# Kernel tuning notes

Measured on AMD Instinct MI355X. Metric: run time of the kernel, lower is better.

## Reference

```python
import jax, jax.numpy as jnp
import numpy as np

B, N, H = 16, 1024, 1024


def setup_inputs() -> dict:
    key = jax.random.key(0)
    ks = jax.random.split(key, 12)
    inv = 1.0 / np.sqrt(H)
    inp = {
        "x": jax.random.normal(ks[0], (B, N, H), jnp.float32),
        "atom_graph": jax.random.normal(ks[1], (B, N, N), jnp.float32),
        "variable_graph": jax.random.normal(ks[2], (B, N, N), jnp.float32),
        "Wq": jax.random.uniform(ks[3], (H, H), jnp.float32, -inv, inv),
        "bq": jax.random.uniform(ks[4], (H,), jnp.float32, -inv, inv),
        "Wk": jax.random.uniform(ks[5], (H, H), jnp.float32, -inv, inv),
        "bk": jax.random.uniform(ks[6], (H,), jnp.float32, -inv, inv),
        "Wv": jax.random.uniform(ks[7], (H, H), jnp.float32, -inv, inv),
        "bv": jax.random.uniform(ks[8], (H,), jnp.float32, -inv, inv),
        "predicate_pos": jax.random.randint(ks[9], (B, N), 0, 2, jnp.int32),
        "variable_tags": jax.random.randint(ks[10], (B, N), 0, 4, jnp.int32),
    }
    return inp


def _path_pool(h, predicate_pos):
    # h: [B,N,H]; predicate_pos: [B,N] in {0,1}
    b, n, d = h.shape
    i = jnp.arange(n)
    # pos[i-2] (value irrelevant for i<2, those branches handled explicitly)
    pp2 = jnp.pad(predicate_pos, ((0, 0), (2, 0)))[:, :n]  # [B,N]
    # window [s, e): i==0 -> [0,2); i==1 -> [0,3); pos[i-2]==1 -> [i,i+2); else [i-1,i+2)
    s = jnp.where(i < 2, 0, jnp.where(pp2 == 1, i, i - 1))  # [B,N]
    e = jnp.where(i == 0, 2, jnp.where(i == 1, 3, i + 2))    # [N]
    e = jnp.minimum(e, n)
    e = jnp.broadcast_to(e, (b, n))
    # prefix sums along node dim with a leading zero row -> windowed means via gather
    cs = jnp.concatenate([jnp.zeros((b, 1, d), h.dtype), jnp.cumsum(h, axis=1)], axis=1)  # [B,N+1,H]
    win_sum = (jnp.take_along_axis(cs, e[:, :, None], axis=1)
               - jnp.take_along_axis(cs, s[:, :, None], axis=1))  # [B,N,H]
    means = win_sum / (e - s)[:, :, None].astype(h.dtype)
    mask = (predicate_pos == 1).astype(h.dtype)  # [B,N]
    item = (means * mask[:, :, None]).sum(axis=1) / mask.sum(axis=1)[:, None]  # [B,H]
    return jnp.broadcast_to(item[:, None, :], (b, n, d))


def reference(x, atom_graph, variable_graph, Wq, bq, Wk, bk, Wv, bv,
              predicate_pos, variable_tags):
    scale = x.shape[-1] ** (-0.5)
    q = (x @ Wq.T + bq) * scale
    k = x @ Wk.T + bk
    v = x @ Wv.T + bv
    att = jnp.einsum("bnh,bmh->bnm", q, k) + atom_graph + variable_graph
    att = jax.nn.softmax(att, axis=-1)  # dropout is identity in eval
    h = jnp.einsum("bnm,bmh->bnh", att, v)
    return _path_pool(h, predicate_pos)
```

## Files before the change

### kernel.cpp

```cpp
#include <hip/hip_runtime.h>
#include <hip/hip_bf16.h>

#define BATCH 16
#define SEQ   1024
#define DIM   1024

typedef __attribute__((ext_vector_type(8))) short bf16x8;
typedef __attribute__((ext_vector_type(4))) float f32x4;
typedef __attribute__((ext_vector_type(4))) unsigned short us4;

__device__ __forceinline__ float bfu2f(unsigned short u) {
  union { unsigned int i; float f; } c; c.i = ((unsigned int)u) << 16; return c.f;
}
__device__ __forceinline__ unsigned short f2bfu(float f) {
  union { float f; unsigned int i; } c; c.f = f;
  return (unsigned short)((c.i + 0x7FFFu + ((c.i >> 16) & 1u)) >> 16);
}
__device__ __forceinline__ void async16(void* lds, const void* g) {
  __builtin_amdgcn_global_load_lds(
      (const __attribute__((address_space(1))) unsigned int*)g,
      (__attribute__((address_space(3))) unsigned int*)lds, 16, 0, 0);
}

__global__ void cast_xw_kernel(const float* __restrict__ x, const float* __restrict__ Wv,
                               unsigned short* __restrict__ xb,
                               unsigned short* __restrict__ Wvb, int x4) {
  int i = blockIdx.x * blockDim.x + threadIdx.x;
  const float* in; unsigned short* out; int j;
  if (i < x4) { in = x; out = xb; j = i; }
  else { in = Wv; out = Wvb; j = i - x4; }
  f32x4 v = ((const f32x4*)in)[j];
  us4 o;
  o[0] = f2bfu(v[0]); o[1] = f2bfu(v[1]); o[2] = f2bfu(v[2]); o[3] = f2bfu(v[3]);
  ((us4*)out)[j] = o;
}

__global__ void castT_kernel(const float* __restrict__ Wq, const float* __restrict__ Wk,
                             unsigned short* __restrict__ WqT,
                             unsigned short* __restrict__ WkT) {
  const float* in = (blockIdx.z == 0) ? Wq : Wk;
  unsigned short* out = (blockIdx.z == 0) ? WqT : WkT;
  __shared__ float t[64][65];
  const int h0 = blockIdx.x * 64, i0 = blockIdx.y * 64;
  const int tid = threadIdx.x;
  const int sub = tid >> 4, c4 = tid & 15;
#pragma unroll
  for (int p = 0; p < 4; ++p) {
    const int row = p * 16 + sub;
    f32x4 v = *(const f32x4*)(in + (size_t)(h0 + row) * DIM + i0 + c4 * 4);
    t[row][c4 * 4 + 0] = v[0]; t[row][c4 * 4 + 1] = v[1];
    t[row][c4 * 4 + 2] = v[2]; t[row][c4 * 4 + 3] = v[3];
  }
  __syncthreads();
#pragma unroll
  for (int p = 0; p < 4; ++p) {
    const int orow = p * 16 + sub;
    us4 o;
    o[0] = f2bfu(t[c4 * 4 + 0][orow]);
    o[1] = f2bfu(t[c4 * 4 + 1][orow]);
    o[2] = f2bfu(t[c4 * 4 + 2][orow]);
    o[3] = f2bfu(t[c4 * 4 + 3][orow]);
    *(us4*)(out + (size_t)(i0 + orow) * DIM + h0 + c4 * 4) = o;
  }
}

__global__ void t12_kernel(const unsigned short* __restrict__ WqT,
                           const unsigned short* __restrict__ WkT,
                           const float* __restrict__ bq, const float* __restrict__ bk,
                           float* __restrict__ t1, float* __restrict__ t2) {
  const int y = blockIdx.y;
  const unsigned short* Wt = y ? WkT : WqT;
  const float* vec = y ? bq : bk;
  float* tout = y ? t2 : t1;
  const int wave = threadIdx.x >> 6, lane = threadIdx.x & 63;
  const int i = blockIdx.x * 4 + wave;
  const us4* wr = (const us4*)(Wt + (size_t)i * DIM);
  float s = 0.f;
#pragma unroll
  for (int t = 0; t < 4; ++t) {
    us4 w4 = wr[lane + 64 * t];
    f32x4 b4 = *(const f32x4*)(vec + (lane + 64 * t) * 4);
    s += bfu2f(w4[0]) * b4[0] + bfu2f(w4[1]) * b4[1] +
         bfu2f(w4[2]) * b4[2] + bfu2f(w4[3]) * b4[3];
  }
#pragma unroll
  for (int o = 32; o; o >>= 1) s += __shfl_down(s, o);
  if (lane == 0) tout[i] = s;
}

__global__ void ac_kernel(const unsigned short* __restrict__ xb,
                          const float* __restrict__ t1, const float* __restrict__ t2,
                          const float* __restrict__ bq, const float* __restrict__ bk,
                          float* __restrict__ a, float* __restrict__ c) {
  const float scale = 0.03125f;
  const int tid = threadIdx.x;
  const int wave = tid >> 6, lane = tid & 63;
  float dp = 0.f;
  for (int i = tid; i < DIM; i += 256) dp += bq[i] * bk[i];
#pragma unroll
  for (int o = 32; o; o >>= 1) dp += __shfl_down(dp, o);
  __shared__ float dred[4];
  if ((tid & 63) == 0) dred[tid >> 6] = dp;
  __syncthreads();
  const float d = dred[0] + dred[1] + dred[2] + dred[3];
  float t1r[16], t2r[16];
#pragma unroll
  for (int t = 0; t < 4; ++t) {
    f32x4 v1 = *(const f32x4*)(t1 + (lane + 64 * t) * 4);
    f32x4 v2 = *(const f32x4*)(t2 + (lane + 64 * t) * 4);
#pragma unroll
    for (int j = 0; j < 4; ++j) { t1r[t * 4 + j] = v1[j]; t2r[t * 4 + j] = v2[j]; }
  }
  for (int rr = 0; rr < 16; ++rr) {
    const int row = blockIdx.x * 64 + wave * 16 + rr;
    const us4* xr = (const us4*)(xb + (size_t)row * DIM);
    float sa = 0.f, sc = 0.f;
#pragma unroll
    for (int t = 0; t < 4; ++t) {
      us4 v = xr[lane + 64 * t];
#pragma unroll
      for (int j = 0; j < 4; ++j) {
        const float f = bfu2f(v[j]);
        sa += f * t1r[t * 4 + j];
        sc += f * t2r[t * 4 + j];
      }
    }
#pragma unroll
    for (int o = 32; o; o >>= 1) { sa += __shfl_down(sa, o); sc += __shfl_down(sc, o); }
    if (lane == 0) {
      a[row] = scale * (sa + d);
      c[row] = scale * sc;
    }
  }
}

__global__ void pathw_kernel(const int* __restrict__ pos, float* __restrict__ w,
                             float* __restrict__ zbias) {
  const int b = blockIdx.x;
  __shared__ int ps[SEQ];
  __shared__ int mcnt;
  const int tid = threadIdx.x;
  if (tid == 0) mcnt = 0;
  __syncthreads();
  if (b == 0)
    for (int i = tid; i < DIM; i += 256) zbias[i] = 0.f;
  for (int i = tid; i < SEQ; i += 256) ps[i] = pos[b * SEQ + i];
  __syncthreads();
  int c = 0;
  for (int i = tid; i < SEQ; i += 256) c += ps[i];
  for (int o = 32; o; o >>= 1) c += __shfl_down(c, o);
  if ((tid & 63) == 0) atomicAdd(&mcnt, c);
  __syncthreads();
  const float invM = 1.0f / (float)mcnt;
  for (int j = tid; j < SEQ; j += 256) {
    float a = 0.f;
#pragma unroll
    for (int di = -1; di <= 1; ++di) {
      int i = j + di;
      if (i < 0 || i >= SEQ) continue;
      if (!ps[i]) continue;
      int s, e;
      if (i < 2) { s = 0; e = (i == 0) ? 2 : 3; }
      else { s = (ps[i - 2] == 1) ? i : (i - 1); e = i + 2; if (e > SEQ) e = SEQ; }
      if (s <= j && j < e) a += 1.0f / (float)(e - s);
    }
    w[b * SEQ + j] = a * invM;
  }
}

__global__ void proj_gemm(const unsigned short* __restrict__ A,
                          const unsigned short* __restrict__ W,
                          const float* __restrict__ bias, float alpha,
                          unsigned short* __restrict__ C, int M, int N, int K)
{
  __shared__ __align__(16) char smem[32768];
  float* Sl = (float*)smem;
  const int tid = threadIdx.x;
  const int wave = tid >> 6, lane = tid & 63;
  const int lr = lane & 15, lg = lane >> 4;
  const int wr = wave >> 1, wc = wave & 1;
  const int flat = blockIdx.x + gridDim.x * blockIdx.y;
  const int q8 = (gridDim.x * gridDim.y) >> 3;
  const int t = (flat & 7) * q8 + (flat >> 3);
  const int m0 = (t / gridDim.y) * 128;
  const int n0 = (t % gridDim.y) * 128;
  const int off0 = tid * 16, off1 = 4096 + tid * 16;
  const int r0 = off0 >> 6, ke0 = (off0 >> 1) & 31;
  const int r1 = off1 >> 6, ke1 = (off1 >> 1) & 31;
  f32x4 acc[4][4] = {};

  auto stage = [&](char* base, int kk) {
    async16(base + off0, A + (size_t)(m0 + r0) * K + kk + ke0);
    async16(base + off1, A + (size_t)(m0 + r1) * K + kk + ke1);
    async16(base + 8192 + off0, W + (size_t)(n0 + r0) * K + kk + ke0);
    async16(base + 8192 + off1, W + (size_t)(n0 + r1) * K + kk + ke1);
  };
  auto compute = [&](const char* base) {
    bf16x8 af[4], bfv[4];
#pragma unroll
    for (int i = 0; i < 4; ++i) {
      af[i]  = *(const bf16x8*)(base + ((wr * 64 + i * 16 + lr) << 6) + (lg << 4));
      bfv[i] = *(const bf16x8*)(base + 8192 + ((wc * 64 + i * 16 + lr) << 6) + (lg << 4));
    }
#pragma unroll
    for (int i = 0; i < 4; ++i)
#pragma unroll
      for (int j = 0; j < 4; ++j)
        acc[i][j] = __builtin_amdgcn_mfma_f32_16x16x32_bf16(af[i], bfv[j], acc[i][j], 0, 0, 0);
  };

  const int nt = K >> 5;
  stage(smem, 0);
  __syncthreads();
  int cur = 0;
  for (int k = 0; k < nt - 1; ++k) {
    stage(smem + ((cur ^ 1) << 14), (k + 1) << 5);
    compute(smem + (cur << 14));
    __syncthreads();
    cur ^= 1;
  }
  compute(smem + (cur << 14));
#pragma unroll
  for (int p = 0; p < 4; ++p) {
    __syncthreads();
    if (wr == (p >> 1)) {
      const int ibase = (p & 1) * 2;
#pragma unroll
      for (int ii = 0; ii < 2; ++ii) {
        const int i = ibase + ii;
#pragma unroll
        for (int j = 0; j < 4; ++j)
#pragma unroll
          for (int r = 0; r < 4; ++r)
            Sl[(ii * 16 + lg * 4 + r) * 132 + wc * 64 + j * 16 + lr] = acc[i][j][r];
      }
    }
    __syncthreads();
#pragma unroll
    for (int it = 0; it < 4; ++it) {
      const int v = tid + it * 256;
      const int lrow = v >> 5, c4 = v & 31;
      const int grow = m0 + p * 32 + lrow;
      const int col = n0 + c4 * 4;
      const f32x4 s4 = *(const f32x4*)(&Sl[lrow * 132 + c4 * 4]);
      const f32x4 b4 = *(const f32x4*)(bias + col);
      us4 o;
      o[0] = f2bfu((s4[0] + b4[0]) * alpha);
      o[1] = f2bfu((s4[1] + b4[1]) * alpha);
      o[2] = f2bfu((s4[2] + b4[2]) * alpha);
      o[3] = f2bfu((s4[3] + b4[3]) * alpha);
      *(us4*)(C + (size_t)grow * N + col) = o;
    }
  }
}

__global__ void sgemm_kernel(const unsigned short* __restrict__ z,
                             const unsigned short* __restrict__ xb,
                             unsigned short* __restrict__ S)
{
  __shared__ __align__(16) char smem[33792];
  unsigned short* Slb = (unsigned short*)smem;
  const int flat = blockIdx.x + 8 * blockIdx.y + 64 * blockIdx.z;
  const int t = (flat & 7) * 128 + (flat >> 3);
  const int b = t >> 6;
  const int m0 = (t & 7) * 128;
  const int n0 = ((t >> 3) & 7) * 128;
  const unsigned short* Aq = z + ((size_t)b << 20);
  const unsigned short* Bk = xb + ((size_t)b << 20);
  const int tid = threadIdx.x;
  const int wave = tid >> 6, lane = tid & 63;
  const int lr = lane & 15, lg = lane >> 4;
  const int wr = wave >> 1, wc = wave & 1;
  const int off0 = tid * 16, off1 = 4096 + tid * 16;
  const int r0 = off0 >> 6, ke0 = (off0 >> 1) & 31;
  const int r1 = off1 >> 6, ke1 = (off1 >> 1) & 31;
  f32x4 acc[4][4] = {};

  auto stage = [&](char* base, int kk) {
    async16(base + off0, Aq + (size_t)(m0 + r0) * DIM + kk + ke0);
    async16(base + off1, Aq + (size_t)(m0 + r1) * DIM + kk + ke1);
    async16(base + 8192 + off0, Bk + (size_t)(n0 + r0) * DIM + kk + ke0);
    async16(base + 8192 + off1, Bk + (size_t)(n0 + r1) * DIM + kk + ke1);
  };
  auto compute = [&](const char* base) {
    bf16x8 af[4], bfv[4];
#pragma unroll
    for (int i = 0; i < 4; ++i) {
      af[i]  = *(const bf16x8*)(base + ((wr * 64 + i * 16 + lr) << 6) + (lg << 4));
      bfv[i] = *(const bf16x8*)(base + 8192 + ((wc * 64 + i * 16 + lr) << 6) + (lg << 4));
    }
#pragma unroll
    for (int i = 0; i < 4; ++i)
#pragma unroll
      for (int j = 0; j < 4; ++j)
        acc[i][j] = __builtin_amdgcn_mfma_f32_16x16x32_bf16(af[i], bfv[j], acc[i][j], 0, 0, 0);
  };

  stage(smem, 0);
  __syncthreads();
  int cur = 0;
  for (int k = 0; k < 31; ++k) {
    stage(smem + ((cur ^ 1) << 14), (k + 1) << 5);
    compute(smem + (cur << 14));
    __syncthreads();
    cur ^= 1;
  }
  compute(smem + (cur << 14));
  __syncthreads();
#pragma unroll
  for (int i = 0; i < 4; ++i)
#pragma unroll
    for (int j = 0; j < 4; ++j)
#pragma unroll
      for (int r = 0; r < 4; ++r)
        Slb[(wr * 64 + i * 16 + lg * 4 + r) * 132 + wc * 64 + j * 16 + lr] =
            f2bfu(acc[i][j][r]);
  __syncthreads();
  unsigned short* Sb = S + ((size_t)b << 20);
#pragma unroll
  for (int it = 0; it < 16; ++it) {
    const int v = tid + it * 256;
    const int lrow = v >> 5, c4 = v & 31;
    *(us4*)(Sb + (size_t)(m0 + lrow) * SEQ + n0 + c4 * 4) =
        *(const us4*)(&Slb[lrow * 132 + c4 * 4]);
  }
}

__global__ void exp_kernel(unsigned short* __restrict__ SE,
                           const float* __restrict__ ag, const float* __restrict__ vg,
                           const float* __restrict__ av, const float* __restrict__ cv,
                           float* __restrict__ denom)
{
  const int b = blockIdx.y;
  const int wave = threadIdx.x >> 6, lane = threadIdx.x & 63;
  const int r0 = blockIdx.x * 8 + wave * 2;
  const float* agb = ag + ((size_t)b << 20);
  const float* vgb = vg + ((size_t)b << 20);
  const float* cvb = cv + b * SEQ;
  unsigned short* Eb = SE + ((size_t)b << 20);
#pragma unroll
  for (int r = 0; r < 2; ++r) {
    const int row = r0 + r;
    const float arow = av[b * SEQ + row];
    us4 sv[4]; f32x4 a4[4], g4[4], cq[4];
#pragma unroll
    for (int qi = 0; qi < 4; ++qi) {
      const int col = (lane + 64 * qi) * 4;
      const size_t base = (size_t)row * SEQ + col;
      sv[qi] = *(const us4*)(Eb + base);
      a4[qi] = *(const f32x4*)(agb + base);
      g4[qi] = *(const f32x4*)(vgb + base);
      cq[qi] = *(const f32x4*)(cvb + col);
    }
    float rs = 0.f;
#pragma unroll
    for (int qi = 0; qi < 4; ++qi) {
      const int col = (lane + 64 * qi) * 4;
      const size_t base = (size_t)row * SEQ + col;
      const float e0 = __expf(bfu2f(sv[qi][0]) + a4[qi][0] + g4[qi][0] + arow + cq[qi][0]);
      const float e1 = __expf(bfu2f(sv[qi][1]) + a4[qi][1] + g4[qi][1] + arow + cq[qi][1]);
      const float e2 = __expf(bfu2f(sv[qi][2]) + a4[qi][2] + g4[qi][2] + arow + cq[qi][2]);
      const float e3 = __expf(bfu2f(sv[qi][3]) + a4[qi][3] + g4[qi][3] + arow + cq[qi][3]);
      us4 o;
      o[0] = f2bfu(e0); o[1] = f2bfu(e1); o[2] = f2bfu(e2); o[3] = f2bfu(e3);
      *(us4*)(Eb + base) = o;
      rs += e0 + e1 + e2 + e3;
    }
#pragma unroll
    for (int o2 = 32; o2; o2 >>= 1) rs += __shfl_down(rs, o2);
    if (lane == 0) denom[b * SEQ + row] = rs;
  }
}

__global__ void wcol_kernel(const unsigned short* __restrict__ Mt,
                            const float* __restrict__ wv,
                            const float* __restrict__ dv,
                            float* __restrict__ part) {
  const int nc = blockIdx.x;
  const int b = blockIdx.y;
  const int tid = threadIdx.x;
  __shared__ float c[64];
  if (tid < 64) {
    const int n = nc * 64 + tid;
    float cvw = wv[b * SEQ + n];
    if (dv) cvw /= dv[b * SEQ + n];
    c[tid] = cvw;
  }
  __syncthreads();
  const unsigned short* p = Mt + ((size_t)b << 20) + ((size_t)(nc * 64) << 10) + tid * 4;
  f32x4 acc = {0.f, 0.f, 0.f, 0.f};
#pragma unroll 8
  for (int n = 0; n < 64; ++n) {
    const us4 v = *(const us4*)(p + ((size_t)n << 10));
    const float cn = c[n];
    acc[0] += cn * bfu2f(v[0]); acc[1] += cn * bfu2f(v[1]);
    acc[2] += cn * bfu2f(v[2]); acc[3] += cn * bfu2f(v[3]);
  }
  *(f32x4*)(part + (size_t)((b * 16 + nc) << 10) + tid * 4) = acc;
}

__global__ void wred_kernel(const float* __restrict__ part, float* __restrict__ vec,
                            float* __restrict__ su) {
  const int b = blockIdx.x;
  const int tid = threadIdx.x;
  f32x4 s = {0.f, 0.f, 0.f, 0.f};
#pragma unroll
  for (int nc = 0; nc < 16; ++nc) {
    const f32x4 v = *(const f32x4*)(part + (size_t)((b * 16 + nc) << 10) + tid * 4);
    s[0] += v[0]; s[1] += v[1]; s[2] += v[2]; s[3] += v[3];
  }
  *(f32x4*)(vec + b * SEQ + tid * 4) = s;
  if (su) {
    float ts = s[0] + s[1] + s[2] + s[3];
#pragma unroll
    for (int o = 32; o; o >>= 1) ts += __shfl_down(ts, o);
    __shared__ float red[4];
    if ((tid & 63) == 0) red[tid >> 6] = ts;
    __syncthreads();
    if (tid == 0) su[b] = red[0] + red[1] + red[2] + red[3];
  }
}

__global__ void item_kernel(const float* __restrict__ y, const float* __restrict__ su,
                            const unsigned short* __restrict__ Wvb,
                            const float* __restrict__ bv, float* __restrict__ item) {
  const int b = blockIdx.x;
  const int hblk = blockIdx.y;
  __shared__ float ys[DIM];
  const int tid = threadIdx.x;
  for (int i = tid; i < DIM; i += 256) ys[i] = y[b * DIM + i];
  __syncthreads();
  const float sub = su[b];
  const int wave = tid >> 6, lane = tid & 63;
  const int h = hblk * 4 + wave;
  const us4* wrow = (const us4*)(Wvb + (size_t)h * DIM);
  float acc = 0.f;
#pragma unroll
  for (int t = 0; t < 4; ++t) {
    us4 v = wrow[t * 64 + lane];
    const int d0 = (t * 64 + lane) * 4;
    acc += ys[d0] * bfu2f(v[0]) + ys[d0 + 1] * bfu2f(v[1]) +
           ys[d0 + 2] * bfu2f(v[2]) + ys[d0 + 3] * bfu2f(v[3]);
  }
  for (int o = 32; o; o >>= 1) acc += __shfl_down(acc, o);
  if (lane == 0) item[b * DIM + h] = acc + sub * bv[h];
}

__global__ void bcast_kernel(const float* __restrict__ item, float* __restrict__ out) {
  const int b = blockIdx.y;
  const int n = blockIdx.x;
  const f32x4* src = (const f32x4*)(item + b * DIM);
  f32x4* dst = (f32x4*)(out + (((size_t)b * SEQ + n) << 10));
  dst[threadIdx.x] = src[threadIdx.x];
}

extern "C" void kernel_launch(void* const* d_in, const int* in_sizes, int n_in,
                              void* d_out, int out_size, void* d_ws, size_t ws_size,
                              hipStream_t stream) {
  const float* x    = (const float*)d_in[0];
  const float* ag   = (const float*)d_in[1];
  const float* vgr  = (const float*)d_in[2];
  const float* Wq   = (const float*)d_in[3];
  const float* bq   = (const float*)d_in[4];
  const float* Wk   = (const float*)d_in[5];
  const float* bk   = (const float*)d_in[6];
  const float* Wv   = (const float*)d_in[7];
  const float* bv   = (const float*)d_in[8];
  const int*   pos  = (const int*)d_in[9];
  float* out = (float*)d_out;

  char* ws = (char*)d_ws;
  size_t off = 0;
  auto alloc = [&](size_t bytes) { void* p = ws + off; off += (bytes + 255) & ~(size_t)255; return p; };
  const size_t BNH = (size_t)BATCH * SEQ * DIM;
  unsigned short* xb   = (unsigned short*)alloc(BNH * 2);
  unsigned short* zb   = (unsigned short*)alloc(BNH * 2);
  unsigned short* E    = (unsigned short*)alloc(BNH * 2);
  unsigned short* WqT  = (unsigned short*)alloc((size_t)DIM * DIM * 2);
  unsigned short* WkT  = (unsigned short*)alloc((size_t)DIM * DIM * 2);
  unsigned short* Wvb  = (unsigned short*)alloc((size_t)DIM * DIM * 2);
  unsigned short* Hb   = (unsigned short*)alloc((size_t)DIM * DIM * 2);
  float* w     = (float*)alloc((size_t)BATCH * SEQ * 4);
  float* denom = (float*)alloc((size_t)BATCH * SEQ * 4);
  float* u     = (float*)alloc((size_t)BATCH * SEQ * 4);
  float* av    = (float*)alloc((size_t)BATCH * SEQ * 4);
  float* cvv   = (float*)alloc((size_t)BATCH * SEQ * 4);
  float* t1    = (float*)alloc((size_t)DIM * 4);
  float* t2    = (float*)alloc((size_t)DIM * 4);
  float* zbias = (float*)alloc((size_t)DIM * 4);
  float* y     = (float*)alloc((size_t)BATCH * DIM * 4);
  float* su    = (float*)alloc((size_t)BATCH * 4);
  float* item  = (float*)alloc((size_t)BATCH * DIM * 4);
  float* part  = (float*)alloc((size_t)BATCH * 16 * SEQ * 4);

  const float scale = 0.03125f;
  const int x4 = (int)(BNH / 4);

  cast_xw_kernel<<<(x4 + DIM * DIM / 4) / 256, 256, 0, stream>>>(x, Wv, xb, Wvb, x4);
  castT_kernel<<<dim3(16, 16, 2), 256, 0, stream>>>(Wq, Wk, WqT, WkT);

  pathw_kernel<<<BATCH, 256, 0, stream>>>(pos, w, zbias);

  t12_kernel<<<dim3(256, 2), 256, 0, stream>>>(WqT, WkT, bq, bk, t1, t2);
  ac_kernel<<<256, 256, 0, stream>>>(xb, t1, t2, bq, bk, av, cvv);

  proj_gemm<<<dim3(8, 8), 256, 0, stream>>>(WkT, WqT, zbias, scale, Hb, DIM, DIM, DIM);

  proj_gemm<<<dim3(128, 8), 256, 0, stream>>>(xb, Hb, zbias, 1.0f, zb,
                                              BATCH * SEQ, DIM, DIM);

  sgemm_kernel<<<dim3(8, 8, BATCH), 256, 0, stream>>>(zb, xb, E);

  exp_kernel<<<dim3(128, BATCH), 256, 0, stream>>>(E, ag, vgr, av, cvv, denom);

  wcol_kernel<<<dim3(16, BATCH), 256, 0, stream>>>(E, w, denom, part);
  wred_kernel<<<BATCH, 256, 0, stream>>>(part, u, su);

  wcol_kernel<<<dim3(16, BATCH), 256, 0, stream>>>(xb, u, nullptr, part);
  wred_kernel<<<BATCH, 256, 0, stream>>>(part, y, nullptr);

  item_kernel<<<dim3(BATCH, 256), 256, 0, stream>>>(y, su, Wvb, bv, item);

  bcast_kernel<<<dim3(SEQ, BATCH), 256, 0, stream>>>(item, out);
}
```

Measured before the change: 223.5 us.

## Fuse softmax exp with weighted column reduction and skip zero-weight rows

```diff
diff --git a/kernel.cpp b/kernel.cpp
--- a/kernel.cpp
+++ b/kernel.cpp
@@ -135,7 +135,7 @@
 }
 
 __global__ void pathw_kernel(const int* __restrict__ pos, float* __restrict__ w,
-                             float* __restrict__ zbias) {
+                             float* __restrict__ u, float* __restrict__ zbias) {
   const int b = blockIdx.x;
   __shared__ int ps[SEQ];
   __shared__ int mcnt;
@@ -144,7 +144,10 @@
   __syncthreads();
   if (b == 0)
     for (int i = tid; i < DIM; i += 256) zbias[i] = 0.f;
-  for (int i = tid; i < SEQ; i += 256) ps[i] = pos[b * SEQ + i];
+  for (int i = tid; i < SEQ; i += 256) {
+    ps[i] = pos[b * SEQ + i];
+    u[b * SEQ + i] = 0.f;
+  }
   __syncthreads();
   int c = 0;
   for (int i = tid; i < SEQ; i += 256) c += ps[i];
@@ -326,66 +329,86 @@
   }
 }
 
-__global__ void exp_kernel(unsigned short* __restrict__ SE,
-                           const float* __restrict__ ag, const float* __restrict__ vg,
-                           const float* __restrict__ av, const float* __restrict__ cv,
-                           float* __restrict__ denom)
+__global__ void exp_fused_kernel(const unsigned short* __restrict__ S,
+                                 const float* __restrict__ ag, const float* __restrict__ vg,
+                                 const float* __restrict__ av, const float* __restrict__ cv,
+                                 const float* __restrict__ w, float* __restrict__ u)
 {
+  __shared__ float uacc[4][SEQ];
   const int b = blockIdx.y;
-  const int wave = threadIdx.x >> 6, lane = threadIdx.x & 63;
-  const int r0 = blockIdx.x * 8 + wave * 2;
+  const int tid = threadIdx.x;
+  const int wave = tid >> 6, lane = tid & 63;
+  for (int i = tid; i < 4 * SEQ; i += 256) ((float*)uacc)[i] = 0.f;
+  __syncthreads();
   const float* agb = ag + ((size_t)b << 20);
   const float* vgb = vg + ((size_t)b << 20);
+  const unsigned short* Sb = S + ((size_t)b << 20);
   const float* cvb = cv + b * SEQ;
-  unsigned short* Eb = SE + ((size_t)b << 20);
+  f32x4 cq[4];
+#pragma unroll
+  for (int qi = 0; qi < 4; ++qi)
+    cq[qi] = *(const f32x4*)(cvb + (lane + 64 * qi) * 4);
+  const int r0 = blockIdx.x * 8 + wave * 2;
 #pragma unroll
   for (int r = 0; r < 2; ++r) {
     const int row = r0 + r;
+    const float wrow = w[b * SEQ + row];
+    if (wrow == 0.f) continue;
     const float arow = av[b * SEQ + row];
-    us4 sv[4]; f32x4 a4[4], g4[4], cq[4];
+    us4 sv[4]; f32x4 a4[4], g4[4];
+#pragma unroll
+    for (int qi = 0; qi < 4; ++qi) {
+      const size_t base = (size_t)row * SEQ + (lane + 64 * qi) * 4;
+      sv[qi] = *(const us4*)(Sb + base);
+      a4[qi] = *(const f32x4*)(agb + base);
+      g4[qi] = *(const f32x4*)(vgb + base);
+    }
+    float e[16];
+    float rs = 0.f;
+#pragma unroll
+    for (int qi = 0; qi < 4; ++qi)
+#pragma unroll
+      for (int j = 0; j < 4; ++j) {
+        const float ev = __expf(bfu2f(sv[qi][j]) + a4[qi][j] + g4[qi][j] + arow + cq[qi][j]);
+        e[qi * 4 + j] = ev;
+        rs += ev;
+      }
+#pragma unroll
+    for (int o2 = 32; o2; o2 >>= 1) rs += __shfl_xor(rs, o2);
+    const float cn = wrow / rs;
 #pragma unroll
     for (int qi = 0; qi < 4; ++qi) {
       const int col = (lane + 64 * qi) * 4;
-      const size_t base = (size_t)row * SEQ + col;
-      sv[qi] = *(const us4*)(Eb + base);
-      a4[qi] = *(const f32x4*)(agb + base);
-      g4[qi] = *(const f32x4*)(vgb + base);
-      cq[qi] = *(const f32x4*)(cvb + col);
-    }
-    float rs = 0.f;
-#pragma unroll
-    for (int qi = 0; qi < 4; ++qi) {
-      const int col = (lane + 64 * qi) * 4;
-      const size_t base = (size_t)row * SEQ + col;
-      const float e0 = __expf(bfu2f(sv[qi][0]) + a4[qi][0] + g4[qi][0] + arow + cq[qi][0]);
-      const float e1 = __expf(bfu2f(sv[qi][1]) + a4[qi][1] + g4[qi][1] + arow + cq[qi][1]);
-      const float e2 = __expf(bfu2f(sv[qi][2]) + a4[qi][2] + g4[qi][2] + arow + cq[qi][2]);
-      const float e3 = __expf(bfu2f(sv[qi][3]) + a4[qi][3] + g4[qi][3] + arow + cq[qi][3]);
-      us4 o;
-      o[0] = f2bfu(e0); o[1] = f2bfu(e1); o[2] = f2bfu(e2); o[3] = f2bfu(e3);
-      *(us4*)(Eb + base) = o;
-      rs += e0 + e1 + e2 + e3;
-    }
-#pragma unroll
-    for (int o2 = 32; o2; o2 >>= 1) rs += __shfl_down(rs, o2);
-    if (lane == 0) denom[b * SEQ + row] = rs;
-  }
+#pragma unroll
+      for (int j = 0; j < 4; ++j)
+        uacc[wave][col + j] += cn * e[qi * 4 + j];
+    }
+  }
+  __syncthreads();
+  const int col = tid * 4;
+  f32x4 s0 = *(const f32x4*)(&uacc[0][col]);
+  const f32x4 s1 = *(const f32x4*)(&uacc[1][col]);
+  const f32x4 s2 = *(const f32x4*)(&uacc[2][col]);
+  const f32x4 s3 = *(const f32x4*)(&uacc[3][col]);
+  s0[0] += s1[0] + s2[0] + s3[0];
+  s0[1] += s1[1] + s2[1] + s3[1];
+  s0[2] += s1[2] + s2[2] + s3[2];
+  s0[3] += s1[3] + s2[3] + s3[3];
+  float* ub = u + b * SEQ + col;
+  atomicAdd(ub + 0, s0[0]);
+  atomicAdd(ub + 1, s0[1]);
+  atomicAdd(ub + 2, s0[2]);
+  atomicAdd(ub + 3, s0[3]);
 }
 
 __global__ void wcol_kernel(const unsigned short* __restrict__ Mt,
                             const float* __restrict__ wv,
-                            const float* __restrict__ dv,
                             float* __restrict__ part) {
   const int nc = blockIdx.x;
   const int b = blockIdx.y;
   const int tid = threadIdx.x;
   __shared__ float c[64];
-  if (tid < 64) {
-    const int n = nc * 64 + tid;
-    float cvw = wv[b * SEQ + n];
-    if (dv) cvw /= dv[b * SEQ + n];
-    c[tid] = cvw;
-  }
+  if (tid < 64) c[tid] = wv[b * SEQ + nc * 64 + tid];
   __syncthreads();
   const unsigned short* p = Mt + ((size_t)b << 20) + ((size_t)(nc * 64) << 10) + tid * 4;
   f32x4 acc = {0.f, 0.f, 0.f, 0.f};
@@ -399,8 +422,7 @@
   *(f32x4*)(part + (size_t)((b * 16 + nc) << 10) + tid * 4) = acc;
 }
 
-__global__ void wred_kernel(const float* __restrict__ part, float* __restrict__ vec,
-                            float* __restrict__ su) {
+__global__ void wred_kernel(const float* __restrict__ part, float* __restrict__ vec) {
   const int b = blockIdx.x;
   const int tid = threadIdx.x;
   f32x4 s = {0.f, 0.f, 0.f, 0.f};
@@ -410,18 +432,9 @@
     s[0] += v[0]; s[1] += v[1]; s[2] += v[2]; s[3] += v[3];
   }
   *(f32x4*)(vec + b * SEQ + tid * 4) = s;
-  if (su) {
-    float ts = s[0] + s[1] + s[2] + s[3];
-#pragma unroll
-    for (int o = 32; o; o >>= 1) ts += __shfl_down(ts, o);
-    __shared__ float red[4];
-    if ((tid & 63) == 0) red[tid >> 6] = ts;
-    __syncthreads();
-    if (tid == 0) su[b] = red[0] + red[1] + red[2] + red[3];
-  }
-}
-
-__global__ void item_kernel(const float* __restrict__ y, const float* __restrict__ su,
+}
+
+__global__ void item_kernel(const float* __restrict__ y,
                             const unsigned short* __restrict__ Wvb,
                             const float* __restrict__ bv, float* __restrict__ item) {
   const int b = blockIdx.x;
@@ -430,7 +443,6 @@
   const int tid = threadIdx.x;
   for (int i = tid; i < DIM; i += 256) ys[i] = y[b * DIM + i];
   __syncthreads();
-  const float sub = su[b];
   const int wave = tid >> 6, lane = tid & 63;
   const int h = hblk * 4 + wave;
   const us4* wrow = (const us4*)(Wvb + (size_t)h * DIM);
@@ -443,7 +455,7 @@
            ys[d0 + 2] * bfu2f(v[2]) + ys[d0 + 3] * bfu2f(v[3]);
   }
   for (int o = 32; o; o >>= 1) acc += __shfl_down(acc, o);
-  if (lane == 0) item[b * DIM + h] = acc + sub * bv[h];
+  if (lane == 0) item[b * DIM + h] = acc + bv[h];
 }
 
 __global__ void bcast_kernel(const float* __restrict__ item, float* __restrict__ out) {
@@ -475,13 +487,12 @@
   const size_t BNH = (size_t)BATCH * SEQ * DIM;
   unsigned short* xb   = (unsigned short*)alloc(BNH * 2);
   unsigned short* zb   = (unsigned short*)alloc(BNH * 2);
-  unsigned short* E    = (unsigned short*)alloc(BNH * 2);
+  unsigned short* S    = (unsigned short*)alloc(BNH * 2);
   unsigned short* WqT  = (unsigned short*)alloc((size_t)DIM * DIM * 2);
   unsigned short* WkT  = (unsigned short*)alloc((size_t)DIM * DIM * 2);
   unsigned short* Wvb  = (unsigned short*)alloc((size_t)DIM * DIM * 2);
   unsigned short* Hb   = (unsigned short*)alloc((size_t)DIM * DIM * 2);
   float* w     = (float*)alloc((size_t)BATCH * SEQ * 4);
-  float* denom = (float*)alloc((size_t)BATCH * SEQ * 4);
   float* u     = (float*)alloc((size_t)BATCH * SEQ * 4);
   float* av    = (float*)alloc((size_t)BATCH * SEQ * 4);
   float* cvv   = (float*)alloc((size_t)BATCH * SEQ * 4);
@@ -489,7 +500,6 @@
   float* t2    = (float*)alloc((size_t)DIM * 4);
   float* zbias = (float*)alloc((size_t)DIM * 4);
   float* y     = (float*)alloc((size_t)BATCH * DIM * 4);
-  float* su    = (float*)alloc((size_t)BATCH * 4);
   float* item  = (float*)alloc((size_t)BATCH * DIM * 4);
   float* part  = (float*)alloc((size_t)BATCH * 16 * SEQ * 4);
 
@@ -499,7 +509,7 @@
   cast_xw_kernel<<<(x4 + DIM * DIM / 4) / 256, 256, 0, stream>>>(x, Wv, xb, Wvb, x4);
   castT_kernel<<<dim3(16, 16, 2), 256, 0, stream>>>(Wq, Wk, WqT, WkT);
 
-  pathw_kernel<<<BATCH, 256, 0, stream>>>(pos, w, zbias);
+  pathw_kernel<<<BATCH, 256, 0, stream>>>(pos, w, u, zbias);
 
   t12_kernel<<<dim3(256, 2), 256, 0, stream>>>(WqT, WkT, bq, bk, t1, t2);
   ac_kernel<<<256, 256, 0, stream>>>(xb, t1, t2, bq, bk, av, cvv);
@@ -509,17 +519,14 @@
   proj_gemm<<<dim3(128, 8), 256, 0, stream>>>(xb, Hb, zbias, 1.0f, zb,
                                               BATCH * SEQ, DIM, DIM);
 
-  sgemm_kernel<<<dim3(8, 8, BATCH), 256, 0, stream>>>(zb, xb, E);
-
-  exp_kernel<<<dim3(128, BATCH), 256, 0, stream>>>(E, ag, vgr, av, cvv, denom);
-
-  wcol_kernel<<<dim3(16, BATCH), 256, 0, stream>>>(E, w, denom, part);
-  wred_kernel<<<BATCH, 256, 0, stream>>>(part, u, su);
-
-  wcol_kernel<<<dim3(16, BATCH), 256, 0, stream>>>(xb, u, nullptr, part);
-  wred_kernel<<<BATCH, 256, 0, stream>>>(part, y, nullptr);
-
-  item_kernel<<<dim3(BATCH, 256), 256, 0, stream>>>(y, su, Wvb, bv, item);
+  sgemm_kernel<<<dim3(8, 8, BATCH), 256, 0, stream>>>(zb, xb, S);
+
+  exp_fused_kernel<<<dim3(128, BATCH), 256, 0, stream>>>(S, ag, vgr, av, cvv, w, u);
+
+  wcol_kernel<<<dim3(16, BATCH), 256, 0, stream>>>(xb, u, part);
+  wred_kernel<<<BATCH, 256, 0, stream>>>(part, y);
+
+  item_kernel<<<dim3(BATCH, 256), 256, 0, stream>>>(y, Wvb, bv, item);
 
   bcast_kernel<<<dim3(SEQ, BATCH), 256, 0, stream>>>(item, out);
 }
```

After: 237.3 us. 6.2% more time.
